# Kernel optimization log

Hardware: AMD Instinct MI355X
Metric: run time of the kernel (lower is better)

Reference implementation:

```python
import jax, jax.numpy as jnp
import numpy as np

B, N, C, H = 2, 2048, 128, 4
C4 = C // 4


def setup_inputs() -> dict:
    key = jax.random.key(0)
    ks = jax.random.split(key, 20)
    s = 0.02
    f = lambda k, sh: (jax.random.normal(k, sh, jnp.float32) * s)
    return {
        'x': jax.random.normal(ks[0], (B, N, C), jnp.float32),
        'A': jax.random.randint(ks[1], (N, N), 0, 2).astype(jnp.int32),
        'q_w1': f(ks[2], (C, C)), 'kv_w1': f(ks[3], (2 * C, C)),
        'proj_w1': f(ks[4], (C, C)), 'proj_b1': jnp.zeros((C,), jnp.float32),
        'q_w2': f(ks[5], (C, C)), 'kv_w2': f(ks[6], (2 * C, C)),
        'proj_w2': f(ks[7], (C, C)), 'proj_b2': jnp.zeros((C,), jnp.float32),
        'cq_w': f(ks[8], (C4, C)), 'cq_b': jnp.zeros((C4,), jnp.float32),
        'ck_w': f(ks[9], (C4, C)), 'ck_b': jnp.zeros((C4,), jnp.float32),
        'cv_w': f(ks[10], (C, C)), 'cv_b': jnp.zeros((C,), jnp.float32),
        'gc_w': f(ks[11], (C, C)), 'gc_b': jnp.zeros((C,), jnp.float32),
    }


def _attn_block(x, A, qw, kvw, pw, pb):
    # Attention._inner_attention + residual; qkv_bias=False, scale=head_dim**-0.5
    b, n, c = x.shape
    hd = c // H
    q = (x @ qw.T).reshape(b, n, H, hd).transpose(0, 2, 1, 3)          # [B,H,N,hd]
    kv = (x @ kvw.T).reshape(b, n, 2, H, hd).transpose(2, 0, 3, 1, 4)  # [2,B,H,N,hd]
    k, v = kv[0], kv[1]
    attn = jnp.einsum('bhnd,bhmd->bhnm', q, k) * (hd ** -0.5)
    attn = jnp.where(A[None, None] > 0, attn, jnp.float32(-9e15))
    attn = jax.nn.softmax(attn, axis=-1)
    out = jnp.einsum('bhnm,bhmd->bhnd', attn, v).transpose(0, 2, 1, 3).reshape(b, n, c)
    return out @ pw.T + pb + x


def _graph_conv(x, cq_w, cq_b, ck_w, ck_b, cv_w, cv_b, gc_w, gc_b):
    # GraphConvolution.forward: conv1d(k=1) QKV, softmax, topk scatter mask, masked softmax, bmm
    b, s, c = x.shape
    xp = x.transpose(0, 2, 1)                                          # [B,C,N]
    query = jnp.einsum('oi,bin->bon', cq_w, xp) + cq_b[:, None]        # [B,C/4,N]
    keyt = (jnp.einsum('oi,bin->bon', ck_w, xp) + ck_b[:, None]).transpose(0, 2, 1)  # [B,N,C/4]
    adj = jax.nn.softmax(jnp.einsum('bnc,bcm->bnm', keyt, query), axis=-1)           # [B,N,N]
    kk = int(s / 3 * 2)                                                # top-2/3 per row
    _, idx = jax.lax.top_k(adj, kk)                                    # [B,N,kk]
    mask = jnp.zeros(adj.shape, bool).at[
        jnp.arange(b)[:, None, None], jnp.arange(s)[None, :, None], idx].set(True)
    adj = jax.nn.softmax(jnp.where(mask, adj, -jnp.inf), axis=-1)
    value = (jnp.einsum('oi,bin->bon', cv_w, xp) + cv_b[:, None]).transpose(0, 2, 1)  # [B,N,C]
    support = value @ gc_w
    return jnp.einsum('bnm,bmc->bnc', adj, support) + gc_b


def reference(x, A, q_w1, kv_w1, proj_w1, proj_b1, q_w2, kv_w2, proj_w2, proj_b2,
              cq_w, cq_b, ck_w, ck_b, cv_w, cv_b, gc_w, gc_b):
    x = _attn_block(x, A, q_w1, kv_w1, proj_w1, proj_b1)
    x = _attn_block(x, A, q_w2, kv_w2, proj_w2, proj_b2)
    return _graph_conv(x, cq_w, cq_b, ck_w, ck_b, cv_w, cv_b, gc_w, gc_b)
```

## Files before the change

kernel.cpp:

```cpp
#include <hip/hip_runtime.h>
#include <hip/hip_bf16.h>
#include <math.h>

#define BB 2
#define NN 2048
#define CC 128
#define HH 4
#define HD 32
#define KK_TOP 1365

typedef __attribute__((ext_vector_type(8))) short v8s;
typedef __attribute__((ext_vector_type(4))) float f32x4;

#define MFMA16(a, b, c) __builtin_amdgcn_mfma_f32_16x16x32_bf16(a, b, c, 0, 0, 0)

__device__ inline float wave_max_f(float v) {
    #pragma unroll
    for (int m = 1; m < 64; m <<= 1) v = fmaxf(v, __shfl_xor(v, m));
    return v;
}
__device__ inline float wave_sum_f(float v) {
    #pragma unroll
    for (int m = 1; m < 64; m <<= 1) v += __shfl_xor(v, m);
    return v;
}
__device__ inline int wave_sum_i(int v) {
    #pragma unroll
    for (int m = 1; m < 64; m <<= 1) v += __shfl_xor(v, m);
    return v;
}
__device__ inline unsigned short bf16bits(float x) {
    __hip_bfloat16 h = __float2bfloat16(x);
    return *reinterpret_cast<unsigned short*>(&h);
}

__global__ __launch_bounds__(256) void packA2_k(const int* __restrict__ A,
                                                unsigned* __restrict__ Ab2)
{
    const int lane = threadIdx.x & 63;
    const int w = threadIdx.x >> 6;
    const int row = blockIdx.x * 4 + w;
    const int* rp = A + (size_t)row * 2048;
    for (int i = 0; i < 32; ++i) {
        unsigned long long bal = __ballot(rp[i * 64 + lane] > 0);
        if (lane == 0)  Ab2[(size_t)row * 64 + 2 * i]     = (unsigned)bal;
        if (lane == 32) Ab2[(size_t)row * 64 + 2 * i + 1] = (unsigned)(bal >> 32);
    }
}

enum { MODE_QKV = 0, MODE_PROJ = 1, MODE_QG = 2, MODE_KG = 3, MODE_SUP = 4 };

template <int MODE>
__global__ __launch_bounds__(256) void gemm128_k(
    const float* __restrict__ X, const float* __restrict__ W0,
    const float* __restrict__ W1, const float* __restrict__ bias,
    const float* __restrict__ resid, void* __restrict__ out0v,
    void* __restrict__ out1v, void* __restrict__ out2v)
{
    __shared__ __align__(16) float Xs[64][132];
    __shared__ __align__(16) float Ws[32][132];
    const int tid = threadIdx.x;
    const int m0 = blockIdx.x * 64;
    const int n0 = blockIdx.y * 32;

    #pragma unroll
    for (int i = 0; i < 32; ++i) {
        int idx = tid + i * 256;
        int row = idx >> 7, col = idx & 127;
        Xs[row][col] = X[(size_t)(m0 + row) * 128 + col];
    }
    #pragma unroll
    for (int i = 0; i < 16; ++i) {
        int idx = tid + i * 256;
        int r = idx >> 7, col = idx & 127;
        int gr = n0 + r;
        const float* wp;
        if (MODE == MODE_QKV)
            wp = (gr < 128) ? (W0 + (size_t)gr * 128) : (W1 + (size_t)(gr - 128) * 128);
        else
            wp = W0 + (size_t)gr * 128;
        Ws[r][col] = wp[col];
    }
    __syncthreads();

    const int r = tid >> 4;
    const int c = tid & 15;
    float acc[4][2] = {{0.f, 0.f}, {0.f, 0.f}, {0.f, 0.f}, {0.f, 0.f}};

    #pragma unroll
    for (int k = 0; k < 128; k += 4) {
        float4 w0 = *(const float4*)&Ws[c][k];
        float4 w1 = *(const float4*)&Ws[c + 16][k];
        #pragma unroll
        for (int i = 0; i < 4; ++i) {
            float4 xv = *(const float4*)&Xs[r + 16 * i][k];
            acc[i][0] += xv.x * w0.x + xv.y * w0.y + xv.z * w0.z + xv.w * w0.w;
            acc[i][1] += xv.x * w1.x + xv.y * w1.y + xv.z * w1.z + xv.w * w1.w;
        }
    }

    #pragma unroll
    for (int i = 0; i < 4; ++i) {
        int m = m0 + r + 16 * i;
        int b = m >> 11, n = m & 2047;
        #pragma unroll
        for (int jj = 0; jj < 2; ++jj) {
            int ccol = n0 + c + 16 * jj;
            float v = acc[i][jj];
            if (MODE == MODE_QKV) {
                __hip_bfloat16 hv = __float2bfloat16(v);
                if (ccol < 128) {
                    int hh = ccol >> 5, d = ccol & 31;
                    ((__hip_bfloat16*)out0v)[((size_t)(b * 4 + hh) * 2048 + n) * 32 + d] = hv;
                } else if (ccol < 256) {
                    int c2 = ccol - 128; int hh = c2 >> 5, d = c2 & 31;
                    ((__hip_bfloat16*)out1v)[((size_t)(b * 4 + hh) * 2048 + n) * 32 + d] = hv;
                } else {
                    int c2 = ccol - 256; int hh = c2 >> 5, d = c2 & 31;
                    ((__hip_bfloat16*)out2v)[((size_t)(b * 4 + hh) * 32 + d) * 2048 + n] = hv;
                }
            } else if (MODE == MODE_PROJ) {
                ((float*)out0v)[(size_t)m * 128 + ccol] = v + bias[ccol] + resid[(size_t)m * 128 + ccol];
            } else if (MODE == MODE_QG) {
                ((float*)out0v)[((size_t)b * 32 + ccol) * 2048 + n] = v + bias[ccol];
            } else if (MODE == MODE_KG) {
                ((float*)out0v)[(size_t)m * 32 + ccol] = v + bias[ccol];
            } else {
                ((__hip_bfloat16*)out0v)[((size_t)b * 128 + ccol) * 2048 + n] = __float2bfloat16(v + bias[ccol]);
            }
        }
    }
}

__global__ __launch_bounds__(256) void attn_mfma_k(
    const short* __restrict__ Qb, const short* __restrict__ Kb,
    const short* __restrict__ Vt, const unsigned* __restrict__ Ab2,
    float* __restrict__ O)
{
    __shared__ __align__(16) float OLDS[4][64][8];
    __shared__ float lred[4][16];

    const int tid = threadIdx.x;
    const int w = tid >> 6, lane = tid & 63;
    const int g = lane >> 4, c = lane & 15;
    const int bb = 4 * g;
    const int wg = blockIdx.x;
    const int b = wg >> 9, h = (wg >> 7) & 3, r0w = (wg & 127) << 4;
    const int bh = b * 4 + h;

    const v8s qf = *(const v8s*)(Qb + ((size_t)bh * 2048 + r0w + c) * 32 + g * 8);
    const short* Kp = Kb + (size_t)bh * 2048 * 32;
    const short* Vp = Vt + (size_t)bh * 32 * 2048;
    const unsigned* Mrow = Ab2 + (size_t)(r0w + c) * 64;

    f32x4 o0 = {0.f, 0.f, 0.f, 0.f}, o1 = {0.f, 0.f, 0.f, 0.f};
    float lsum = 0.f;
    const float SC2 = 0.25503487f;
    const bool lo = (g < 2);
    const int aA = (32 * (g & 1) + c) * 4;
    const int aB = aA + 64;

    #pragma unroll 2
    for (int t = 0; t < 16; ++t) {
        const int kt = t * 4 + w;
        const int key0 = kt * 32;
        v8s kf0 = *(const v8s*)(Kp + (size_t)(key0 + c) * 32 + g * 8);
        v8s kf1 = *(const v8s*)(Kp + (size_t)(key0 + 16 + c) * 32 + g * 8);
        unsigned mw = Mrow[kt];
        const f32x4 z = {0.f, 0.f, 0.f, 0.f};
        f32x4 s0 = MFMA16(kf0, qf, z);
        f32x4 s1 = MFMA16(kf1, qf, z);

        float p0[4], p1[4];
        #pragma unroll
        for (int r = 0; r < 4; ++r) {
            p0[r] = ((mw >> (bb + r)) & 1u)      ? exp2f(s0[r] * SC2) : 0.f;
            p1[r] = ((mw >> (16 + bb + r)) & 1u) ? exp2f(s1[r] * SC2) : 0.f;
        }
        lsum += p0[0] + p0[1] + p0[2] + p0[3] + p1[0] + p1[1] + p1[2] + p1[3];

        int w00 = (int)bf16bits(p0[0]) | ((int)bf16bits(p0[1]) << 16);
        int w01 = (int)bf16bits(p0[2]) | ((int)bf16bits(p0[3]) << 16);
        int w10 = (int)bf16bits(p1[0]) | ((int)bf16bits(p1[1]) << 16);
        int w11 = (int)bf16bits(p1[2]) | ((int)bf16bits(p1[3]) << 16);

        int e0, e1;
        union { int wv[4]; v8s v; } pf;
        e0 = __builtin_amdgcn_ds_bpermute(aA, w00);
        e1 = __builtin_amdgcn_ds_bpermute(aA, w10);
        pf.wv[0] = lo ? e0 : e1;
        e0 = __builtin_amdgcn_ds_bpermute(aA, w01);
        e1 = __builtin_amdgcn_ds_bpermute(aA, w11);
        pf.wv[1] = lo ? e0 : e1;
        e0 = __builtin_amdgcn_ds_bpermute(aB, w00);
        e1 = __builtin_amdgcn_ds_bpermute(aB, w10);
        pf.wv[2] = lo ? e0 : e1;
        e0 = __builtin_amdgcn_ds_bpermute(aB, w01);
        e1 = __builtin_amdgcn_ds_bpermute(aB, w11);
        pf.wv[3] = lo ? e0 : e1;

        v8s vf0 = *(const v8s*)(Vp + (size_t)c * 2048 + key0 + g * 8);
        v8s vf1 = *(const v8s*)(Vp + (size_t)(16 + c) * 2048 + key0 + g * 8);
        o0 = MFMA16(pf.v, vf0, o0);
        o1 = MFMA16(pf.v, vf1, o1);
    }

    lsum += __shfl_xor(lsum, 16);
    lsum += __shfl_xor(lsum, 32);

    *(f32x4*)&OLDS[w][lane][0] = o0;
    *(f32x4*)&OLDS[w][lane][4] = o1;
    if (lane < 16) lred[w][lane] = lsum;
    __syncthreads();

    if (tid < 64) {
        float iv[4];
        #pragma unroll
        for (int r = 0; r < 4; ++r) {
            float s = lred[0][bb + r] + lred[1][bb + r] + lred[2][bb + r] + lred[3][bb + r];
            iv[r] = 1.f / s;
        }
        f32x4 a0 = *(f32x4*)&OLDS[0][lane][0];
        f32x4 a1 = *(f32x4*)&OLDS[0][lane][4];
        #pragma unroll
        for (int ww = 1; ww < 4; ++ww) {
            a0 += *(f32x4*)&OLDS[ww][lane][0];
            a1 += *(f32x4*)&OLDS[ww][lane][4];
        }
        #pragma unroll
        for (int r = 0; r < 4; ++r) {
            size_t base = ((size_t)b * 2048 + r0w + bb + r) * 128 + h * 32;
            O[base + c]      = a0[r] * iv[r];
            O[base + 16 + c] = a1[r] * iv[r];
        }
    }
}

__global__ __launch_bounds__(256) void gadjtopk_k(
    const float* __restrict__ Kg, const float* __restrict__ QgT,
    __hip_bfloat16* __restrict__ ADJb)
{
    __shared__ float kg_s[4][32];
    __shared__ float scores[4][2048];
    __shared__ float redm[4][4], reds[4][4];

    const int tid = threadIdx.x;
    const int wg = blockIdx.x;
    const int b = wg >> 9;
    const int r0 = (wg & 511) << 2;

    if (tid < 128) {
        int rr = tid >> 5, d = tid & 31;
        kg_s[rr][d] = Kg[((size_t)b * 2048 + r0 + rr) * 32 + d];
    }
    __syncthreads();

    const float* Qp = QgT + (size_t)b * 32 * 2048;
    float acc[4][8];
    #pragma unroll
    for (int rr = 0; rr < 4; ++rr)
        #pragma unroll
        for (int s = 0; s < 8; ++s) acc[rr][s] = 0.f;

    #pragma unroll
    for (int d0 = 0; d0 < 32; d0 += 8) {
        float qr[4][8];
        #pragma unroll
        for (int rr = 0; rr < 4; ++rr)
            #pragma unroll
            for (int dd = 0; dd < 8; ++dd) qr[rr][dd] = kg_s[rr][d0 + dd];
        #pragma unroll
        for (int dd = 0; dd < 8; ++dd) {
            const float* kp = Qp + (size_t)(d0 + dd) * 2048 + tid;
            #pragma unroll
            for (int s = 0; s < 8; ++s) {
                float kv = kp[s * 256];
                acc[0][s] = fmaf(qr[0][dd], kv, acc[0][s]);
                acc[1][s] = fmaf(qr[1][dd], kv, acc[1][s]);
                acc[2][s] = fmaf(qr[2][dd], kv, acc[2][s]);
                acc[3][s] = fmaf(qr[3][dd], kv, acc[3][s]);
            }
        }
    }
    #pragma unroll
    for (int s = 0; s < 8; ++s) {
        int jj = tid + 256 * s;
        #pragma unroll
        for (int rr = 0; rr < 4; ++rr) scores[rr][jj] = acc[rr][s];
    }
    __syncthreads();

    const int lane = tid & 63, wid = tid >> 6;
    #pragma unroll
    for (int rr = 0; rr < 4; ++rr) {
        float m = -3.0e38f;
        #pragma unroll
        for (int s = 0; s < 8; ++s) m = fmaxf(m, scores[rr][tid + 256 * s]);
        m = wave_max_f(m);
        if (lane == 0) redm[rr][wid] = m;
    }
    __syncthreads();
    float mx[4];
    #pragma unroll
    for (int rr = 0; rr < 4; ++rr)
        mx[rr] = fmaxf(fmaxf(redm[rr][0], redm[rr][1]), fmaxf(redm[rr][2], redm[rr][3]));
    #pragma unroll
    for (int rr = 0; rr < 4; ++rr) {
        float sm = 0.f;
        #pragma unroll
        for (int s = 0; s < 8; ++s) {
            int jj = tid + 256 * s;
            float p = expf(scores[rr][jj] - mx[rr]);
            scores[rr][jj] = p;
            sm += p;
        }
        sm = wave_sum_f(sm);
        if (lane == 0) reds[rr][wid] = sm;
    }
    __syncthreads();

    const float ivw = 1.f / (reds[wid][0] + reds[wid][1] + reds[wid][2] + reds[wid][3]);
    unsigned k_[32];
    float mxp = 0.f;
    #pragma unroll
    for (int i = 0; i < 32; ++i) {
        float p = scores[wid][lane + i * 64] * ivw;
        k_[i] = __float_as_uint(p);
        mxp = fmaxf(mxp, p);
    }
    mxp = wave_max_f(mxp);

    unsigned thr = 0u;
    for (int bit = 29; bit >= 0; --bit) {
        unsigned cand = thr | (1u << bit);
        int cnt = 0;
        #pragma unroll
        for (int i = 0; i < 32; ++i) cnt += (k_[i] >= cand) ? 1 : 0;
        cnt = wave_sum_i(cnt);
        if (cnt >= KK_TOP) thr = cand;
    }

    int gt_c = 0;
    #pragma unroll
    for (int i = 0; i < 32; ++i) gt_c += (k_[i] > thr) ? 1 : 0;
    gt_c = wave_sum_i(gt_c);
    const int need = KK_TOP - gt_c;

    unsigned keepmask = 0u;
    int running = 0;
    const unsigned long long ltmask = (lane == 0) ? 0ull : (~0ull >> (64 - lane));
    #pragma unroll
    for (int i = 0; i < 32; ++i) {
        bool tie = (k_[i] == thr);
        unsigned long long bal = __ballot(tie);
        int before = running + (int)__popcll(bal & ltmask);
        bool keep = (k_[i] > thr) || (tie && before < need);
        running += (int)__popcll(bal);
        if (keep) keepmask |= (1u << i);
    }

    const float LOG2E = 1.4426950408889634f;
    float sm = 0.f;
    #pragma unroll
    for (int i = 0; i < 32; ++i)
        if ((keepmask >> i) & 1u)
            sm += exp2f((__uint_as_float(k_[i]) - mxp) * LOG2E);
    sm = wave_sum_f(sm);
    const float ivs = 1.f / sm;

    __hip_bfloat16* rp = ADJb + (size_t)(b * 2048 + r0 + wid) * 2048;
    #pragma unroll
    for (int i = 0; i < 32; ++i) {
        float o = ((keepmask >> i) & 1u)
                    ? exp2f((__uint_as_float(k_[i]) - mxp) * LOG2E) * ivs : 0.f;
        rp[lane + i * 64] = __float2bfloat16(o);
    }
}

__global__ __launch_bounds__(256) void fusew_k(
    const float* __restrict__ cv_w, const float* __restrict__ cv_b,
    const float* __restrict__ gc_w, float* __restrict__ MT, float* __restrict__ B2)
{
    int c = blockIdx.x * 2 + (threadIdx.x >> 7);
    int k = threadIdx.x & 127;
    float a = 0.f;
    for (int i = 0; i < 128; ++i) a += cv_w[(size_t)i * 128 + k] * gc_w[(size_t)i * 128 + c];
    MT[(size_t)c * 128 + k] = a;
    if (blockIdx.x == 0 && threadIdx.x < 128) {
        float s = 0.f;
        for (int i = 0; i < 128; ++i) s += cv_b[i] * gc_w[(size_t)i * 128 + threadIdx.x];
        B2[threadIdx.x] = s;
    }
}

__global__ __launch_bounds__(256) void outgemm_mfma_k(
    const short* __restrict__ ADJb, const short* __restrict__ SUPt,
    const float* __restrict__ gcb, float* __restrict__ OUT)
{
    __shared__ __align__(16) float OL[4][64][32];
    const int tid = threadIdx.x;
    const int w = tid >> 6, lane = tid & 63;
    const int g = lane >> 4, c = lane & 15;
    const int r0w = blockIdx.x * 16;
    const int b = r0w >> 11;
    const short* Bp = SUPt + (size_t)b * 128 * 2048;

    f32x4 acc[8];
    #pragma unroll
    for (int f = 0; f < 8; ++f) acc[f] = (f32x4){0.f, 0.f, 0.f, 0.f};

    #pragma unroll 2
    for (int i = 0; i < 16; ++i) {
        const int k0 = w * 512 + i * 32;
        v8s af = *(const v8s*)(ADJb + (size_t)(r0w + c) * 2048 + k0 + g * 8);
        #pragma unroll
        for (int f = 0; f < 8; ++f) {
            v8s bf_ = *(const v8s*)(Bp + (size_t)(f * 16 + c) * 2048 + k0 + g * 8);
            acc[f] = MFMA16(af, bf_, acc[f]);
        }
    }

    #pragma unroll
    for (int f = 0; f < 8; ++f) *(f32x4*)&OL[w][lane][f * 4] = acc[f];
    __syncthreads();

    const int sbase = w * 8;
    #pragma unroll
    for (int u = 0; u < 8; ++u) {
        int s = sbase + u;
        float v = OL[0][lane][s] + OL[1][lane][s] + OL[2][lane][s] + OL[3][lane][s];
        int f = s >> 2, r = s & 3;
        int row = r0w + 4 * g + r;
        int col = f * 16 + c;
        OUT[(size_t)row * 128 + col] = v + gcb[col];
    }
}

extern "C" void kernel_launch(void* const* d_in, const int* in_sizes, int n_in,
                              void* d_out, int out_size, void* d_ws, size_t ws_size,
                              hipStream_t stream)
{
    const float* x       = (const float*)d_in[0];
    const int*   A       = (const int*)d_in[1];
    const float* q_w1    = (const float*)d_in[2];
    const float* kv_w1   = (const float*)d_in[3];
    const float* proj_w1 = (const float*)d_in[4];
    const float* proj_b1 = (const float*)d_in[5];
    const float* q_w2    = (const float*)d_in[6];
    const float* kv_w2   = (const float*)d_in[7];
    const float* proj_w2 = (const float*)d_in[8];
    const float* proj_b2 = (const float*)d_in[9];
    const float* cq_w    = (const float*)d_in[10];
    const float* cq_b    = (const float*)d_in[11];
    const float* ck_w    = (const float*)d_in[12];
    const float* ck_b    = (const float*)d_in[13];
    const float* cv_w    = (const float*)d_in[14];
    const float* cv_b    = (const float*)d_in[15];
    const float* gc_w    = (const float*)d_in[16];
    const float* gc_b    = (const float*)d_in[17];
    float* out = (float*)d_out;

    char* ws = (char*)d_ws;
    __hip_bfloat16* Qb   = (__hip_bfloat16*)(ws + 0);
    __hip_bfloat16* Kb   = (__hip_bfloat16*)(ws + 1048576);
    __hip_bfloat16* Vt   = (__hip_bfloat16*)(ws + 2097152);
    __hip_bfloat16* ADJb = (__hip_bfloat16*)(ws + 3145728);
    unsigned*       Ab2  = (unsigned*)      (ws + 19922944);
    float*          O    = (float*)         (ws + 20447232);
    float*          X1   = (float*)         (ws + 22544384);
    float*          X2   = (float*)         (ws + 24641536);
    float*          QgT  = (float*)         (ws + 26738688);
    float*          Kg   = (float*)         (ws + 27262976);
    __hip_bfloat16* SUPt = (__hip_bfloat16*)(ws + 27787264);
    float*          MT   = (float*)         (ws + 28835840);
    float*          B2   = (float*)         (ws + 28901376);

    dim3 blk(256);

    hipLaunchKernelGGL(packA2_k, dim3(512), blk, 0, stream, A, Ab2);
    hipLaunchKernelGGL(fusew_k, dim3(64), blk, 0, stream, cv_w, cv_b, gc_w, MT, B2);

    hipLaunchKernelGGL((gemm128_k<MODE_QKV>), dim3(64, 12), blk, 0, stream,
                       x, q_w1, kv_w1, nullptr, nullptr, Qb, Kb, Vt);
    hipLaunchKernelGGL(attn_mfma_k, dim3(1024), blk, 0, stream,
                       (const short*)Qb, (const short*)Kb, (const short*)Vt, Ab2, O);
    hipLaunchKernelGGL((gemm128_k<MODE_PROJ>), dim3(64, 4), blk, 0, stream,
                       O, proj_w1, nullptr, proj_b1, x, X1, nullptr, nullptr);

    hipLaunchKernelGGL((gemm128_k<MODE_QKV>), dim3(64, 12), blk, 0, stream,
                       X1, q_w2, kv_w2, nullptr, nullptr, Qb, Kb, Vt);
    hipLaunchKernelGGL(attn_mfma_k, dim3(1024), blk, 0, stream,
                       (const short*)Qb, (const short*)Kb, (const short*)Vt, Ab2, O);
    hipLaunchKernelGGL((gemm128_k<MODE_PROJ>), dim3(64, 4), blk, 0, stream,
                       O, proj_w2, nullptr, proj_b2, X1, X2, nullptr, nullptr);

    hipLaunchKernelGGL((gemm128_k<MODE_QG>), dim3(64, 1), blk, 0, stream,
                       X2, cq_w, nullptr, cq_b, nullptr, QgT, nullptr, nullptr);
    hipLaunchKernelGGL((gemm128_k<MODE_KG>), dim3(64, 1), blk, 0, stream,
                       X2, ck_w, nullptr, ck_b, nullptr, Kg, nullptr, nullptr);
    hipLaunchKernelGGL((gemm128_k<MODE_SUP>), dim3(64, 4), blk, 0, stream,
                       X2, MT, nullptr, B2, nullptr, SUPt, nullptr, nullptr);
    hipLaunchKernelGGL(gadjtopk_k, dim3(1024), blk, 0, stream, Kg, QgT, ADJb);
    hipLaunchKernelGGL(outgemm_mfma_k, dim3(256), blk, 0, stream,
                       (const short*)ADJb, (const short*)SUPt, gc_b, out);
}
```

Before: 318.7 us.

## Merge prep and graph GEMM launches, speed up top-k threshold search, split output GEMM

Merges A-packing and weight fusion into one prep kernel, and the three graph projection GEMMs into one launch, cutting launch count. The top-k radix search now starts from the highest bit where the row min and max differ and counts with ballot/popcount instead of shuffle reductions. Score computation uses contiguous float4 loads, and exponentials are computed once and reused. The output MFMA GEMM is split across two column halves to double block count. The trade-offs are more register use and extra branching in the merged kernels.

```diff
diff --git a/kernel.cpp b/kernel.cpp
--- a/kernel.cpp
+++ b/kernel.cpp
@@ -19,12 +19,12 @@
     for (int m = 1; m < 64; m <<= 1) v = fmaxf(v, __shfl_xor(v, m));
     return v;
 }
+__device__ inline float wave_min_f(float v) {
+    #pragma unroll
+    for (int m = 1; m < 64; m <<= 1) v = fminf(v, __shfl_xor(v, m));
+    return v;
+}
 __device__ inline float wave_sum_f(float v) {
-    #pragma unroll
-    for (int m = 1; m < 64; m <<= 1) v += __shfl_xor(v, m);
-    return v;
-}
-__device__ inline int wave_sum_i(int v) {
     #pragma unroll
     for (int m = 1; m < 64; m <<= 1) v += __shfl_xor(v, m);
     return v;
@@ -34,21 +34,42 @@
     return *reinterpret_cast<unsigned short*>(&h);
 }
 
-__global__ __launch_bounds__(256) void packA2_k(const int* __restrict__ A,
-                                                unsigned* __restrict__ Ab2)
-{
-    const int lane = threadIdx.x & 63;
-    const int w = threadIdx.x >> 6;
-    const int row = blockIdx.x * 4 + w;
-    const int* rp = A + (size_t)row * 2048;
-    for (int i = 0; i < 32; ++i) {
-        unsigned long long bal = __ballot(rp[i * 64 + lane] > 0);
-        if (lane == 0)  Ab2[(size_t)row * 64 + 2 * i]     = (unsigned)bal;
-        if (lane == 32) Ab2[(size_t)row * 64 + 2 * i + 1] = (unsigned)(bal >> 32);
-    }
-}
-
-enum { MODE_QKV = 0, MODE_PROJ = 1, MODE_QG = 2, MODE_KG = 3, MODE_SUP = 4 };
+__global__ __launch_bounds__(256) void prep_k(
+    const int* __restrict__ A, unsigned* __restrict__ Ab2,
+    const float* __restrict__ cv_w, const float* __restrict__ cv_b,
+    const float* __restrict__ gc_w, float* __restrict__ MT, float* __restrict__ B2)
+{
+    const int bx = blockIdx.x;
+    if (bx < 512) {
+        const int lane = threadIdx.x & 63;
+        const int w = threadIdx.x >> 6;
+        const int row = bx * 4 + w;
+        const int* rp = A + (size_t)row * 2048;
+        for (int i = 0; i < 32; ++i) {
+            unsigned long long bal = __ballot(rp[i * 64 + lane] > 0);
+            if (lane == 0)  Ab2[(size_t)row * 64 + 2 * i]     = (unsigned)bal;
+            if (lane == 32) Ab2[(size_t)row * 64 + 2 * i + 1] = (unsigned)(bal >> 32);
+        }
+    } else {
+        const int b2 = bx - 512;
+        const int c = b2 * 2 + (threadIdx.x >> 7);
+        const int k = threadIdx.x & 127;
+        float a = 0.f;
+        #pragma unroll 4
+        for (int i = 0; i < 128; ++i)
+            a += cv_w[(size_t)i * 128 + k] * gc_w[(size_t)i * 128 + c];
+        MT[(size_t)c * 128 + k] = a;
+        if (b2 == 0 && threadIdx.x < 128) {
+            float s = 0.f;
+            #pragma unroll 4
+            for (int i = 0; i < 128; ++i)
+                s += cv_b[i] * gc_w[(size_t)i * 128 + threadIdx.x];
+            B2[threadIdx.x] = s;
+        }
+    }
+}
+
+enum { MODE_QKV = 0, MODE_PROJ = 1 };
 
 template <int MODE>
 __global__ __launch_bounds__(256) void gemm128_k(
@@ -119,14 +140,73 @@
                     int c2 = ccol - 256; int hh = c2 >> 5, d = c2 & 31;
                     ((__hip_bfloat16*)out2v)[((size_t)(b * 4 + hh) * 32 + d) * 2048 + n] = hv;
                 }
-            } else if (MODE == MODE_PROJ) {
+            } else {
                 ((float*)out0v)[(size_t)m * 128 + ccol] = v + bias[ccol] + resid[(size_t)m * 128 + ccol];
-            } else if (MODE == MODE_QG) {
-                ((float*)out0v)[((size_t)b * 32 + ccol) * 2048 + n] = v + bias[ccol];
-            } else if (MODE == MODE_KG) {
-                ((float*)out0v)[(size_t)m * 32 + ccol] = v + bias[ccol];
+            }
+        }
+    }
+}
+
+__global__ __launch_bounds__(256) void graphmm_k(
+    const float* __restrict__ X, const float* __restrict__ cq_w,
+    const float* __restrict__ cq_b, const float* __restrict__ ck_w,
+    const float* __restrict__ ck_b, const float* __restrict__ MT,
+    const float* __restrict__ B2, float* __restrict__ QgT,
+    float* __restrict__ Kg, __hip_bfloat16* __restrict__ SUPt)
+{
+    __shared__ __align__(16) float Xs[64][132];
+    __shared__ __align__(16) float Ws[32][132];
+    const int tid = threadIdx.x;
+    const int m0 = blockIdx.x * 64;
+    const int y = blockIdx.y;
+    const float* W0   = (y == 0) ? cq_w : (y == 1) ? ck_w : MT;
+    const float* bias = (y == 0) ? cq_b : (y == 1) ? ck_b : B2;
+    const int n0 = (y < 2) ? 0 : (y - 2) * 32;
+
+    #pragma unroll
+    for (int i = 0; i < 32; ++i) {
+        int idx = tid + i * 256;
+        int row = idx >> 7, col = idx & 127;
+        Xs[row][col] = X[(size_t)(m0 + row) * 128 + col];
+    }
+    #pragma unroll
+    for (int i = 0; i < 16; ++i) {
+        int idx = tid + i * 256;
+        int r = idx >> 7, col = idx & 127;
+        Ws[r][col] = W0[(size_t)(n0 + r) * 128 + col];
+    }
+    __syncthreads();
+
+    const int r = tid >> 4;
+    const int c = tid & 15;
+    float acc[4][2] = {{0.f, 0.f}, {0.f, 0.f}, {0.f, 0.f}, {0.f, 0.f}};
+
+    #pragma unroll
+    for (int k = 0; k < 128; k += 4) {
+        float4 w0 = *(const float4*)&Ws[c][k];
+        float4 w1 = *(const float4*)&Ws[c + 16][k];
+        #pragma unroll
+        for (int i = 0; i < 4; ++i) {
+            float4 xv = *(const float4*)&Xs[r + 16 * i][k];
+            acc[i][0] += xv.x * w0.x + xv.y * w0.y + xv.z * w0.z + xv.w * w0.w;
+            acc[i][1] += xv.x * w1.x + xv.y * w1.y + xv.z * w1.z + xv.w * w1.w;
+        }
+    }
+
+    #pragma unroll
+    for (int i = 0; i < 4; ++i) {
+        int m = m0 + r + 16 * i;
+        int b = m >> 11, n = m & 2047;
+        #pragma unroll
+        for (int jj = 0; jj < 2; ++jj) {
+            int ccol = n0 + c + 16 * jj;
+            float v = acc[i][jj];
+            if (y == 0) {
+                QgT[((size_t)b * 32 + ccol) * 2048 + n] = v + bias[ccol];
+            } else if (y == 1) {
+                Kg[(size_t)m * 32 + ccol] = v + bias[ccol];
             } else {
-                ((__hip_bfloat16*)out0v)[((size_t)b * 128 + ccol) * 2048 + n] = __float2bfloat16(v + bias[ccol]);
+                SUPt[((size_t)b * 128 + ccol) * 2048 + n] = __float2bfloat16(v + bias[ccol]);
             }
         }
     }
@@ -256,37 +336,40 @@
     __syncthreads();
 
     const float* Qp = QgT + (size_t)b * 32 * 2048;
+    const int ncol = tid * 8;
     float acc[4][8];
     #pragma unroll
     for (int rr = 0; rr < 4; ++rr)
         #pragma unroll
-        for (int s = 0; s < 8; ++s) acc[rr][s] = 0.f;
+        for (int j = 0; j < 8; ++j) acc[rr][j] = 0.f;
 
     #pragma unroll
     for (int d0 = 0; d0 < 32; d0 += 8) {
         float qr[4][8];
         #pragma unroll
-        for (int rr = 0; rr < 4; ++rr)
+        for (int rr = 0; rr < 4; ++rr) {
+            float4 qa = *(const float4*)&kg_s[rr][d0];
+            float4 qb = *(const float4*)&kg_s[rr][d0 + 4];
+            qr[rr][0] = qa.x; qr[rr][1] = qa.y; qr[rr][2] = qa.z; qr[rr][3] = qa.w;
+            qr[rr][4] = qb.x; qr[rr][5] = qb.y; qr[rr][6] = qb.z; qr[rr][7] = qb.w;
+        }
+        #pragma unroll
+        for (int dd = 0; dd < 8; ++dd) {
+            const float* kp = Qp + (size_t)(d0 + dd) * 2048 + ncol;
+            float4 v0 = *(const float4*)kp;
+            float4 v1 = *(const float4*)(kp + 4);
+            float kv[8] = {v0.x, v0.y, v0.z, v0.w, v1.x, v1.y, v1.z, v1.w};
             #pragma unroll
-            for (int dd = 0; dd < 8; ++dd) qr[rr][dd] = kg_s[rr][d0 + dd];
-        #pragma unroll
-        for (int dd = 0; dd < 8; ++dd) {
-            const float* kp = Qp + (size_t)(d0 + dd) * 2048 + tid;
-            #pragma unroll
-            for (int s = 0; s < 8; ++s) {
-                float kv = kp[s * 256];
-                acc[0][s] = fmaf(qr[0][dd], kv, acc[0][s]);
-                acc[1][s] = fmaf(qr[1][dd], kv, acc[1][s]);
-                acc[2][s] = fmaf(qr[2][dd], kv, acc[2][s]);
-                acc[3][s] = fmaf(qr[3][dd], kv, acc[3][s]);
-            }
-        }
-    }
-    #pragma unroll
-    for (int s = 0; s < 8; ++s) {
-        int jj = tid + 256 * s;
-        #pragma unroll
-        for (int rr = 0; rr < 4; ++rr) scores[rr][jj] = acc[rr][s];
+            for (int rr = 0; rr < 4; ++rr)
+                #pragma unroll
+                for (int j = 0; j < 8; ++j)
+                    acc[rr][j] = fmaf(qr[rr][dd], kv[j], acc[rr][j]);
+        }
+    }
+    #pragma unroll
+    for (int rr = 0; rr < 4; ++rr) {
+        *(float4*)&scores[rr][ncol]     = (float4){acc[rr][0], acc[rr][1], acc[rr][2], acc[rr][3]};
+        *(float4*)&scores[rr][ncol + 4] = (float4){acc[rr][4], acc[rr][5], acc[rr][6], acc[rr][7]};
     }
     __syncthreads();
 
@@ -321,29 +404,37 @@
 
     const float ivw = 1.f / (reds[wid][0] + reds[wid][1] + reds[wid][2] + reds[wid][3]);
     unsigned k_[32];
-    float mxp = 0.f;
+    float mxp = 0.f, mnp = 3.0e38f;
     #pragma unroll
     for (int i = 0; i < 32; ++i) {
         float p = scores[wid][lane + i * 64] * ivw;
         k_[i] = __float_as_uint(p);
         mxp = fmaxf(mxp, p);
+        mnp = fminf(mnp, p);
     }
     mxp = wave_max_f(mxp);
-
-    unsigned thr = 0u;
-    for (int bit = 29; bit >= 0; --bit) {
-        unsigned cand = thr | (1u << bit);
-        int cnt = 0;
-        #pragma unroll
-        for (int i = 0; i < 32; ++i) cnt += (k_[i] >= cand) ? 1 : 0;
-        cnt = wave_sum_i(cnt);
-        if (cnt >= KK_TOP) thr = cand;
+    mnp = wave_min_f(mnp);
+
+    unsigned thr = __float_as_uint(mnp);
+    const unsigned umax = __float_as_uint(mxp);
+    const unsigned diff = thr ^ umax;
+    if (diff != 0u) {
+        const int hb = 31 - __builtin_clz(diff);
+        thr = (umax >> (hb + 1)) << (hb + 1);
+        for (int bit = hb; bit >= 0; --bit) {
+            unsigned cand = thr | (1u << bit);
+            int cnt = 0;
+            #pragma unroll
+            for (int i = 0; i < 32; ++i)
+                cnt += (int)__popcll(__ballot(k_[i] >= cand));
+            if (cnt >= KK_TOP) thr = cand;
+        }
     }
 
     int gt_c = 0;
     #pragma unroll
-    for (int i = 0; i < 32; ++i) gt_c += (k_[i] > thr) ? 1 : 0;
-    gt_c = wave_sum_i(gt_c);
+    for (int i = 0; i < 32; ++i)
+        gt_c += (int)__popcll(__ballot(k_[i] > thr));
     const int need = KK_TOP - gt_c;
 
     unsigned keepmask = 0u;
@@ -360,36 +451,22 @@
     }
 
     const float LOG2E = 1.4426950408889634f;
+    float e_[32];
+    #pragma unroll
+    for (int i = 0; i < 32; ++i)
+        e_[i] = exp2f((__uint_as_float(k_[i]) - mxp) * LOG2E);
     float sm = 0.f;
     #pragma unroll
     for (int i = 0; i < 32; ++i)
-        if ((keepmask >> i) & 1u)
-            sm += exp2f((__uint_as_float(k_[i]) - mxp) * LOG2E);
+        sm += ((keepmask >> i) & 1u) ? e_[i] : 0.f;
     sm = wave_sum_f(sm);
     const float ivs = 1.f / sm;
 
     __hip_bfloat16* rp = ADJb + (size_t)(b * 2048 + r0 + wid) * 2048;
     #pragma unroll
     for (int i = 0; i < 32; ++i) {
-        float o = ((keepmask >> i) & 1u)
-                    ? exp2f((__uint_as_float(k_[i]) - mxp) * LOG2E) * ivs : 0.f;
+        float o = ((keepmask >> i) & 1u) ? e_[i] * ivs : 0.f;
         rp[lane + i * 64] = __float2bfloat16(o);
-    }
-}
-
-__global__ __launch_bounds__(256) void fusew_k(
-    const float* __restrict__ cv_w, const float* __restrict__ cv_b,
-    const float* __restrict__ gc_w, float* __restrict__ MT, float* __restrict__ B2)
-{
-    int c = blockIdx.x * 2 + (threadIdx.x >> 7);
-    int k = threadIdx.x & 127;
-    float a = 0.f;
-    for (int i = 0; i < 128; ++i) a += cv_w[(size_t)i * 128 + k] * gc_w[(size_t)i * 128 + c];
-    MT[(size_t)c * 128 + k] = a;
-    if (blockIdx.x == 0 && threadIdx.x < 128) {
-        float s = 0.f;
-        for (int i = 0; i < 128; ++i) s += cv_b[i] * gc_w[(size_t)i * 128 + threadIdx.x];
-        B2[threadIdx.x] = s;
     }
 }
 
@@ -397,41 +474,42 @@
     const short* __restrict__ ADJb, const short* __restrict__ SUPt,
     const float* __restrict__ gcb, float* __restrict__ OUT)
 {
-    __shared__ __align__(16) float OL[4][64][32];
+    __shared__ __align__(16) float OL[4][64][16];
     const int tid = threadIdx.x;
     const int w = tid >> 6, lane = tid & 63;
     const int g = lane >> 4, c = lane & 15;
     const int r0w = blockIdx.x * 16;
+    const int n0 = blockIdx.y * 64;
     const int b = r0w >> 11;
     const short* Bp = SUPt + (size_t)b * 128 * 2048;
 
-    f32x4 acc[8];
-    #pragma unroll
-    for (int f = 0; f < 8; ++f) acc[f] = (f32x4){0.f, 0.f, 0.f, 0.f};
+    f32x4 acc[4];
+    #pragma unroll
+    for (int f = 0; f < 4; ++f) acc[f] = (f32x4){0.f, 0.f, 0.f, 0.f};
 
     #pragma unroll 2
     for (int i = 0; i < 16; ++i) {
         const int k0 = w * 512 + i * 32;
         v8s af = *(const v8s*)(ADJb + (size_t)(r0w + c) * 2048 + k0 + g * 8);
         #pragma unroll
-        for (int f = 0; f < 8; ++f) {
-            v8s bf_ = *(const v8s*)(Bp + (size_t)(f * 16 + c) * 2048 + k0 + g * 8);
+        for (int f = 0; f < 4; ++f) {
+            v8s bf_ = *(const v8s*)(Bp + (size_t)(n0 + f * 16 + c) * 2048 + k0 + g * 8);
             acc[f] = MFMA16(af, bf_, acc[f]);
         }
     }
 
     #pragma unroll
-    for (int f = 0; f < 8; ++f) *(f32x4*)&OL[w][lane][f * 4] = acc[f];
-    __syncthreads();
-
-    const int sbase = w * 8;
-    #pragma unroll
-    for (int u = 0; u < 8; ++u) {
-        int s = sbase + u;
-        float v = OL[0][lane][s] + OL[1][lane][s] + OL[2][lane][s] + OL[3][lane][s];
+    for (int f = 0; f < 4; ++f) *(f32x4*)&OL[w][lane][f * 4] = acc[f];
+    __syncthreads();
+
+    #pragma unroll
+    for (int u = 0; u < 4; ++u) {
+        int idx = tid + u * 256;
+        int ls = idx >> 4, s = idx & 15;
+        float v = OL[0][ls][s] + OL[1][ls][s] + OL[2][ls][s] + OL[3][ls][s];
         int f = s >> 2, r = s & 3;
-        int row = r0w + 4 * g + r;
-        int col = f * 16 + c;
+        int row = r0w + 4 * (ls >> 4) + r;
+        int col = n0 + f * 16 + (ls & 15);
         OUT[(size_t)row * 128 + col] = v + gcb[col];
     }
 }
@@ -477,8 +555,7 @@
 
     dim3 blk(256);
 
-    hipLaunchKernelGGL(packA2_k, dim3(512), blk, 0, stream, A, Ab2);
-    hipLaunchKernelGGL(fusew_k, dim3(64), blk, 0, stream, cv_w, cv_b, gc_w, MT, B2);
+    hipLaunchKernelGGL(prep_k, dim3(576), blk, 0, stream, A, Ab2, cv_w, cv_b, gc_w, MT, B2);
 
     hipLaunchKernelGGL((gemm128_k<MODE_QKV>), dim3(64, 12), blk, 0, stream,
                        x, q_w1, kv_w1, nullptr, nullptr, Qb, Kb, Vt);
@@ -494,13 +571,9 @@
     hipLaunchKernelGGL((gemm128_k<MODE_PROJ>), dim3(64, 4), blk, 0, stream,
                        O, proj_w2, nullptr, proj_b2, X1, X2, nullptr, nullptr);
 
-    hipLaunchKernelGGL((gemm128_k<MODE_QG>), dim3(64, 1), blk, 0, stream,
-                       X2, cq_w, nullptr, cq_b, nullptr, QgT, nullptr, nullptr);
-    hipLaunchKernelGGL((gemm128_k<MODE_KG>), dim3(64, 1), blk, 0, stream,
-                       X2, ck_w, nullptr, ck_b, nullptr, Kg, nullptr, nullptr);
-    hipLaunchKernelGGL((gemm128_k<MODE_SUP>), dim3(64, 4), blk, 0, stream,
-                       X2, MT, nullptr, B2, nullptr, SUPt, nullptr, nullptr);
+    hipLaunchKernelGGL(graphmm_k, dim3(64, 6), blk, 0, stream,
+                       X2, cq_w, cq_b, ck_w, ck_b, MT, B2, QgT, Kg, SUPt);
     hipLaunchKernelGGL(gadjtopk_k, dim3(1024), blk, 0, stream, Kg, QgT, ADJb);
-    hipLaunchKernelGGL(outgemm_mfma_k, dim3(256), blk, 0, stream,
+    hipLaunchKernelGGL(outgemm_mfma_k, dim3(256, 2), blk, 0, stream,
                        (const short*)ADJb, (const short*)SUPt, gc_b, out);
 }
```

Result: faster. 305.8 us (-4.0%).
